# Performance work log

Hardware: AMD Instinct MI355X
Metric: run time of the kernel (lower is better)

Reference implementation:

```python
import jax, jax.numpy as jnp
import numpy as np

EPS = 1e-6

def _l2norm(t):
    # F.normalize over channel axis (axis=1) of (B, dk, L)
    n = jnp.sqrt(jnp.sum(t * t, axis=1, keepdims=True))
    return t / jnp.maximum(n, EPS)

def setup_inputs() -> dict:
    key = jax.random.key(0)
    ks = jax.random.split(key, 8)
    B, Cin, Cenc, dk, dv, H, W = 2, 64, 96, 64, 64, 96, 96
    return {
        "x": jax.random.normal(ks[0], (B, Cin, H, W), dtype=jnp.float32),
        "x_enc": jax.random.normal(ks[1], (B, Cenc, H, W), dtype=jnp.float32),
        "Wq": jax.random.normal(ks[2], (dk, Cenc), dtype=jnp.float32) * 0.05,
        "bq": jax.random.normal(ks[3], (dk,), dtype=jnp.float32) * 0.05,
        "Wk": jax.random.normal(ks[4], (dk, Cenc), dtype=jnp.float32) * 0.05,
        "bk": jax.random.normal(ks[5], (dk,), dtype=jnp.float32) * 0.05,
        "Wv": jax.random.normal(ks[6], (dv, Cin), dtype=jnp.float32) * 0.05,
        "bv": jax.random.normal(ks[7], (dv,), dtype=jnp.float32) * 0.05,
    }

def reference(x, x_enc, Wq, bq, Wk, bk, Wv, bv):
    B, _, H, W = x.shape
    L = H * W
    # 1x1 conv projections == channel matmuls, then flatten spatial dims
    Q = (jnp.einsum('bchw,kc->bkhw', x_enc, Wq) + bq[None, :, None, None]).reshape(B, -1, L)
    K = (jnp.einsum('bchw,kc->bkhw', x_enc, Wk) + bk[None, :, None, None]).reshape(B, -1, L)
    V = (jnp.einsum('bchw,kc->bkhw', x, Wv) + bv[None, :, None, None]).reshape(B, -1, L)
    # per-position L2 normalization over the dk channel axis ('l2' mode)
    Q = _l2norm(Q)
    K = _l2norm(K)
    # A[b,i,j] = sum_q Q[b,q,i] * K[b,q,j], softmax over j
    A = jax.nn.softmax(jnp.einsum('bqi,bqj->bij', Q, K), axis=-1)  # (B, L, L)
    R = jnp.einsum('bij,bvj->bvi', A, V)  # (B, dv, L)
    return R.reshape(B, -1, H, W)
```

## Files before the change

kernel.cpp:

```cpp
#include <hip/hip_runtime.h>
#include <hip/hip_bf16.h>
#include <math.h>

#define NB   2
#define CIN  64
#define CENC 96
#define DK   64
#define DV   64
#define LL   9216
#define QBLK 256
#define KVBLK 64
#define NQT  (LL/QBLK)
#define LOG2E 1.44269504088896340736f

typedef __attribute__((ext_vector_type(8)))  short short8;
typedef __attribute__((ext_vector_type(16))) float f32x16;
typedef __attribute__((ext_vector_type(2)))  unsigned int uint2v;
typedef unsigned int uint;

__device__ inline void gload16(const void* g, void* l) {
    __builtin_amdgcn_global_load_lds(
        (const __attribute__((address_space(1))) unsigned int*)g,
        (__attribute__((address_space(3))) unsigned int*)l, 16, 0, 0);
}

__device__ inline unsigned short f2bf(float f) {
    union { float f; uint u; } v; v.f = f;
    uint r = (v.u + 0x7FFFu + ((v.u >> 16) & 1u)) >> 16;
    return (unsigned short)r;
}

__device__ inline float bf2f(uint u) {
    union { uint u; float f; } c; c.u = u << 16; return c.f;
}

__device__ inline uint cvtpk(float lo, float hi) {
    uint r;
    asm("v_cvt_pk_bf16_f32 %0, %1, %2" : "=v"(r) : "v"(lo), "v"(hi));
    return r;
}

__device__ inline void plswap(uint& a, uint& b) {
#if __has_builtin(__builtin_amdgcn_permlane32_swap)
    uint2v r = __builtin_amdgcn_permlane32_swap(a, b, false, false);
    a = r.x; b = r.y;
#else
    const int lane = threadIdx.x & 63;
    uint t = (lane < 32) ? b : a;
    t = __shfl_xor(t, 32, 64);
    uint an = (lane < 32) ? a : t;
    uint bn = (lane < 32) ? t : b;
    a = an; b = bn;
#endif
}

__global__ __launch_bounds__(256) void proj_kernel(
    const float* __restrict__ x, const float* __restrict__ x_enc,
    const float* __restrict__ Wq, const float* __restrict__ bq,
    const float* __restrict__ Wk, const float* __restrict__ bk,
    const float* __restrict__ Wv, const float* __restrict__ bv,
    unsigned short* __restrict__ Qb, unsigned short* __restrict__ Kb,
    unsigned short* __restrict__ Vt, int nqk)
{
    __shared__ float sh[2 * CENC * 64];
    const int tid = threadIdx.x;

    if ((int)blockIdx.x < nqk) {
        float* Wt0 = sh;
        float* Wt1 = sh + CENC * 64;
        for (int idx = tid; idx < DK * CENC; idx += 256) {
            int k = idx / CENC, c = idx - k * CENC;
            Wt0[c * 64 + (k ^ (c & 31))] = Wq[idx];
            Wt1[c * 64 + (k ^ (c & 31))] = Wk[idx];
        }
        __syncthreads();

        const int w    = __builtin_amdgcn_readfirstlane(tid >> 6);
        const int lane = tid & 63;
        const int gw   = blockIdx.x * 4 + w;
        const int p0g  = gw * 16;
        const int b    = p0g / LL;
        const int p0   = p0g - b * LL;

        float qa[16], ka[16];
        const float bqv = bq[lane], bkv = bk[lane];
#pragma unroll
        for (int p = 0; p < 16; ++p) { qa[p] = bqv; ka[p] = bkv; }

        const float* xp = x_enc + (size_t)b * CENC * LL + p0;
#pragma unroll 4
        for (int c = 0; c < CENC; ++c) {
            const float wq = Wt0[c * 64 + (lane ^ (c & 31))];
            const float wk = Wt1[c * 64 + (lane ^ (c & 31))];
            const float* xc = xp + (size_t)c * LL;
#pragma unroll
            for (int p = 0; p < 16; ++p) {
                const float xv = xc[p];
                qa[p] = fmaf(wq, xv, qa[p]);
                ka[p] = fmaf(wk, xv, ka[p]);
            }
        }

        unsigned short* qrow = Qb + (size_t)(b * LL + p0) * 64 + lane;
        unsigned short* krow = Kb + (size_t)(b * LL + p0) * 64 + lane;
#pragma unroll
        for (int p = 0; p < 16; ++p) {
            float sq = qa[p] * qa[p];
            float sk = ka[p] * ka[p];
#pragma unroll
            for (int m = 1; m < 64; m <<= 1) {
                sq += __shfl_xor(sq, m, 64);
                sk += __shfl_xor(sk, m, 64);
            }
            qrow[(size_t)p * 64] = f2bf(qa[p] * (LOG2E / fmaxf(sqrtf(sq), 1e-6f)));
            krow[(size_t)p * 64] = f2bf(ka[p] * (1.f / fmaxf(sqrtf(sk), 1e-6f)));
        }
    } else {
        float* Wt = sh;
        unsigned short* Vsh = (unsigned short*)(sh + CIN * 64);
        for (int idx = tid; idx < DV * CIN; idx += 256) {
            int v = idx / CIN, c = idx - v * CIN;
            Wt[c * 64 + (v ^ (c & 31))] = Wv[idx];
        }
        __syncthreads();

        const int w    = __builtin_amdgcn_readfirstlane(tid >> 6);
        const int lane = tid & 63;
        const int l0g  = ((int)blockIdx.x - nqk) * 64;
        const int b    = l0g / LL;
        const int l0   = l0g - b * LL;
        const int p0   = w * 16;

        float va[16];
        const float bvv = bv[lane];
#pragma unroll
        for (int p = 0; p < 16; ++p) va[p] = bvv;

        const float* xp = x + (size_t)b * CIN * LL + l0 + p0;
#pragma unroll 4
        for (int c = 0; c < CIN; ++c) {
            const float wv = Wt[c * 64 + (lane ^ (c & 31))];
            const float* xc = xp + (size_t)c * LL;
#pragma unroll
            for (int p = 0; p < 16; ++p) va[p] = fmaf(wv, xc[p], va[p]);
        }
#pragma unroll
        for (int p = 0; p < 16; ++p) Vsh[(p0 + p) * 64 + lane] = f2bf(va[p]);
        __syncthreads();

        const int v = tid & 63, w2 = tid >> 6;
        uint pk[8];
#pragma unroll
        for (int j = 0; j < 8; ++j)
            pk[j] = (uint)Vsh[(w2 * 16 + 2 * j) * 64 + v] |
                    ((uint)Vsh[(w2 * 16 + 2 * j + 1) * 64 + v] << 16);
        uint4* dst = (uint4*)(Vt + (size_t)b * 64 * LL + (size_t)v * LL + l0 + w2 * 16);
        dst[0] = make_uint4(pk[0], pk[1], pk[2], pk[3]);
        dst[1] = make_uint4(pk[4], pk[5], pk[6], pk[7]);
    }
}

__global__ __launch_bounds__(256, 2) void flash_kernel(
    const unsigned short* __restrict__ Qb,
    const unsigned short* __restrict__ Kb,
    const unsigned short* __restrict__ Vt,
    float* __restrict__ Sp, unsigned short* __restrict__ Rp,
    int JS, int nt)
{
    __shared__ unsigned short Sh[16384];

    const int bid0  = blockIdx.x;
    const int chunk = gridDim.x >> 3;
    const int bid   = (bid0 & 7) * chunk + (bid0 >> 3);

    const int qt  = bid % NQT;
    const int js  = (bid / NQT) % JS;
    const int b   = bid / (NQT * JS);
    const int tid = threadIdx.x;
    const int w = tid >> 6, lane = tid & 63;
    const int ln = lane & 31, h = lane >> 5;
    const int i0w = qt * QBLK + w * 64;

    short8 qf[2][4];
#pragma unroll
    for (int ig = 0; ig < 2; ++ig)
#pragma unroll
        for (int kc = 0; kc < 4; ++kc)
            qf[ig][kc] = *(const short8*)(Qb + ((size_t)(b * LL + i0w + ig * 32 + ln)) * 64 + kc * 16 + h * 8);

    int aK[4];
#pragma unroll
    for (int kc = 0; kc < 4; ++kc)
        aK[kc] = ln * 128 + ((((kc << 1) + h) ^ (ln & 7)) << 4);

    const int o0 = w * 1024 + lane * 16;
    const int r0 = o0 >> 7;
    const int c0 = ((o0 >> 4) & 7) ^ (r0 & 7);

    const unsigned short* KbB = Kb + (size_t)b * LL * 64;
    const unsigned short* VtB = Vt + (size_t)b * 64 * LL;
    const int jbase = js * nt * KVBLK;

    f32x16 racc[2][2];
#pragma unroll
    for (int ig = 0; ig < 2; ++ig)
#pragma unroll
        for (int vg = 0; vg < 2; ++vg)
#pragma unroll
            for (int r = 0; r < 16; ++r) racc[ig][vg][r] = 0.f;
    float ssum[2] = {0.f, 0.f};

    gload16(KbB + (size_t)(jbase + r0) * 64 + c0 * 8, (char*)Sh + w * 1024);
    gload16(KbB + (size_t)(jbase + 32 + r0) * 64 + c0 * 8, (char*)Sh + 4096 + w * 1024);
    gload16(VtB + (size_t)r0 * LL + jbase + c0 * 8, (char*)Sh + 16384 + w * 1024);
    gload16(VtB + (size_t)(32 + r0) * LL + jbase + c0 * 8, (char*)Sh + 16384 + 4096 + w * 1024);

    const unsigned short* pK = KbB + (size_t)(jbase + KVBLK + r0) * 64 + c0 * 8;
    const unsigned short* pV = VtB + (size_t)r0 * LL + jbase + KVBLK + c0 * 8;

#define PREF(BUFOFF)                                                            \
    do {                                                                        \
        gload16(pK,                    (char*)Sh + (BUFOFF) + w * 1024);        \
        gload16(pK + 32 * 64,          (char*)Sh + (BUFOFF) + 4096 + w * 1024); \
        gload16(pV,                    (char*)Sh + 16384 + (BUFOFF) + w * 1024);\
        gload16(pV + (size_t)32 * LL,  (char*)Sh + 16384 + (BUFOFF) + 4096 + w * 1024); \
        pK += KVBLK * 64; pV += KVBLK;                                          \
    } while (0)

#define COMPUTE(BUFOFF)                                                         \
    do {                                                                        \
        _Pragma("unroll")                                                       \
        for (int jt = 0; jt < 2; ++jt) {                                        \
            f32x16 sacc[2];                                                     \
            _Pragma("unroll")                                                   \
            for (int ig = 0; ig < 2; ++ig)                                      \
                _Pragma("unroll")                                               \
                for (int r = 0; r < 16; ++r) sacc[ig][r] = 0.f;                 \
            __builtin_amdgcn_s_setprio(1);                                      \
            _Pragma("unroll")                                                   \
            for (int kc = 0; kc < 4; ++kc) {                                    \
                const short8 kf = *(const short8*)((const char*)Sh + (BUFOFF) + jt * 4096 + aK[kc]); \
                sacc[0] = __builtin_amdgcn_mfma_f32_32x32x16_bf16(kf, qf[0][kc], sacc[0], 0, 0, 0); \
                sacc[1] = __builtin_amdgcn_mfma_f32_32x32x16_bf16(kf, qf[1][kc], sacc[1], 0, 0, 0); \
            }                                                                   \
            __builtin_amdgcn_s_setprio(0);                                      \
            short8 pf[2][2];                                                    \
            _Pragma("unroll")                                                   \
            for (int ig = 0; ig < 2; ++ig) {                                    \
                _Pragma("unroll")                                               \
                for (int r = 0; r < 16; ++r) sacc[ig][r] = __builtin_amdgcn_exp2f(sacc[ig][r]); \
                float s0 = 0.f;                                                 \
                _Pragma("unroll")                                               \
                for (int r = 0; r < 16; r += 4)                                 \
                    s0 += (sacc[ig][r] + sacc[ig][r + 1]) + (sacc[ig][r + 2] + sacc[ig][r + 3]); \
                ssum[ig] += s0;                                                 \
                _Pragma("unroll")                                               \
                for (int c = 0; c < 2; ++c) {                                   \
                    uint a0 = cvtpk(sacc[ig][8 * c + 0], sacc[ig][8 * c + 1]);  \
                    uint b0 = cvtpk(sacc[ig][8 * c + 4], sacc[ig][8 * c + 5]);  \
                    uint a1 = cvtpk(sacc[ig][8 * c + 2], sacc[ig][8 * c + 3]);  \
                    uint b1 = cvtpk(sacc[ig][8 * c + 6], sacc[ig][8 * c + 7]);  \
                    plswap(a0, b0);                                             \
                    plswap(a1, b1);                                             \
                    union { uint u[4]; short8 s; } P;                           \
                    P.u[0] = a0; P.u[1] = a1; P.u[2] = b0; P.u[3] = b1;         \
                    pf[ig][c] = P.s;                                            \
                }                                                               \
            }                                                                   \
            __builtin_amdgcn_s_setprio(1);                                      \
            _Pragma("unroll")                                                   \
            for (int c = 0; c < 2; ++c) {                                       \
                const int kcv = 2 * jt + c;                                     \
                _Pragma("unroll")                                               \
                for (int vg = 0; vg < 2; ++vg) {                                \
                    const short8 vf = *(const short8*)((const char*)Sh + 16384 + (BUFOFF) + vg * 4096 + aK[kcv]); \
                    racc[0][vg] = __builtin_amdgcn_mfma_f32_32x32x16_bf16(pf[0][c], vf, racc[0][vg], 0, 0, 0); \
                    racc[1][vg] = __builtin_amdgcn_mfma_f32_32x32x16_bf16(pf[1][c], vf, racc[1][vg], 0, 0, 0); \
                }                                                               \
            }                                                                   \
            __builtin_amdgcn_s_setprio(0);                                      \
        }                                                                       \
    } while (0)

    int t = 0;
    for (; t + 2 <= nt; t += 2) {
        __syncthreads();
        PREF(8192);
        COMPUTE(0);
        __syncthreads();
        if (t + 2 < nt) PREF(0);
        COMPUTE(8192);
    }
    if (t < nt) {
        __syncthreads();
        COMPUTE(0);
    }
#undef PREF
#undef COMPUTE

#pragma unroll
    for (int ig = 0; ig < 2; ++ig) {
        float s = ssum[ig] + __shfl_xor(ssum[ig], 32, 64);
        if (h == 0) Sp[(size_t)(b * JS + js) * LL + i0w + ig * 32 + ln] = s;
    }
    const size_t rBase = (size_t)(b * JS + js) * 64;
#pragma unroll
    for (int ig = 0; ig < 2; ++ig)
#pragma unroll
        for (int vg = 0; vg < 2; ++vg) {
            unsigned short* dst = Rp + (rBase + vg * 32 + ln) * (size_t)LL + i0w + ig * 32 + 4 * h;
#pragma unroll
            for (int rr = 0; rr < 4; ++rr) {
                uint2v val;
                val.x = cvtpk(racc[ig][vg][4 * rr + 0], racc[ig][vg][4 * rr + 1]);
                val.y = cvtpk(racc[ig][vg][4 * rr + 2], racc[ig][vg][4 * rr + 3]);
                *(uint2v*)&dst[8 * rr] = val;
            }
        }
}

__global__ __launch_bounds__(256) void combine_kernel(
    const float* __restrict__ Sp, const unsigned short* __restrict__ Rp,
    float* __restrict__ out, int JS)
{
    size_t g4 = ((size_t)blockIdx.x * 256 + threadIdx.x) * 4;
    int l = (int)(g4 % LL);
    int v = (int)((g4 / LL) % 64);
    int b = (int)(g4 / ((size_t)64 * LL));
    float4 s = make_float4(0.f, 0.f, 0.f, 0.f);
    float4 r = make_float4(0.f, 0.f, 0.f, 0.f);
    for (int js = 0; js < JS; ++js) {
        const float4 sv = *(const float4*)&Sp[(size_t)(b * JS + js) * LL + l];
        const uint2v rv = *(const uint2v*)&Rp[((size_t)(b * JS + js) * 64 + v) * LL + l];
        s.x += sv.x; s.y += sv.y; s.z += sv.z; s.w += sv.w;
        r.x += bf2f(rv.x & 0xffffu); r.y += bf2f(rv.x >> 16);
        r.z += bf2f(rv.y & 0xffffu); r.w += bf2f(rv.y >> 16);
    }
    *(float4*)&out[g4] = make_float4(r.x / s.x, r.y / s.y, r.z / s.z, r.w / s.w);
}

extern "C" void kernel_launch(void* const* d_in, const int* in_sizes, int n_in,
                              void* d_out, int out_size, void* d_ws, size_t ws_size,
                              hipStream_t stream) {
    (void)in_sizes; (void)n_in; (void)out_size;
    const float* x     = (const float*)d_in[0];
    const float* x_enc = (const float*)d_in[1];
    const float* Wq    = (const float*)d_in[2];
    const float* bq    = (const float*)d_in[3];
    const float* Wk    = (const float*)d_in[4];
    const float* bk    = (const float*)d_in[5];
    const float* Wv    = (const float*)d_in[6];
    const float* bv    = (const float*)d_in[7];
    float* out = (float*)d_out;
    char* ws = (char*)d_ws;

    const size_t nBF = (size_t)NB * LL * 64 * 2;
    unsigned short* Qb = (unsigned short*)ws;
    unsigned short* Kb = (unsigned short*)(ws + nBF);
    unsigned short* Vt = (unsigned short*)(ws + 2 * nBF);

    int JS = 8;
    {
        const int cand[3] = {16, 12, 8};
        for (int ci = 0; ci < 3; ++ci) {
            JS = cand[ci];
            size_t need = 3 * nBF + (size_t)NB * JS * LL * 4 + (size_t)NB * JS * 64 * LL * 2;
            if (need <= ws_size) break;
        }
    }
    float* Sp = (float*)(ws + 3 * nBF);
    unsigned short* Rp = (unsigned short*)(ws + 3 * nBF + (size_t)NB * JS * LL * 4);
    int nt = (LL / JS) / KVBLK;

    const int nqk = NB * LL / 64;
    proj_kernel   <<<2 * nqk, 256, 0, stream>>>(x, x_enc, Wq, bq, Wk, bk, Wv, bv, Qb, Kb, Vt, nqk);
    flash_kernel  <<<NB * JS * NQT, 256, 0, stream>>>(Qb, Kb, Vt, Sp, Rp, JS, nt);
    combine_kernel<<<(NB * 64 * LL) / 1024, 256, 0, stream>>>(Sp, Rp, out, JS);
}
```

Baseline: 98.12 us.

## Double KV tile to 128 keys per stage and reduce split-K count

Raises the key/value block from 64 to 128 rows per pipeline stage, doubling the shared-memory buffers to 64 KB and processing four 32-key subtiles per stage. This halves the number of barriers and prefetch issues per block. The KV split factor drops from 16 to 12, so each block runs longer and there are fewer partial results for the combine kernel. The larger LDS footprint may limit how many blocks fit per CU, and fewer blocks in the grid lowers parallelism.

```diff
diff --git a/kernel.cpp b/kernel.cpp
--- a/kernel.cpp
+++ b/kernel.cpp
@@ -9,7 +9,7 @@
 #define DV   64
 #define LL   9216
 #define QBLK 256
-#define KVBLK 64
+#define KVBLK 128
 #define NQT  (LL/QBLK)
 #define LOG2E 1.44269504088896340736f
 
@@ -167,7 +167,7 @@
     float* __restrict__ Sp, unsigned short* __restrict__ Rp,
     int JS, int nt)
 {
-    __shared__ unsigned short Sh[16384];
+    __shared__ unsigned short Sh[32768];
 
     const int bid0  = blockIdx.x;
     const int chunk = gridDim.x >> 3;
@@ -210,76 +210,86 @@
             for (int r = 0; r < 16; ++r) racc[ig][vg][r] = 0.f;
     float ssum[2] = {0.f, 0.f};
 
-    gload16(KbB + (size_t)(jbase + r0) * 64 + c0 * 8, (char*)Sh + w * 1024);
-    gload16(KbB + (size_t)(jbase + 32 + r0) * 64 + c0 * 8, (char*)Sh + 4096 + w * 1024);
-    gload16(VtB + (size_t)r0 * LL + jbase + c0 * 8, (char*)Sh + 16384 + w * 1024);
-    gload16(VtB + (size_t)(32 + r0) * LL + jbase + c0 * 8, (char*)Sh + 16384 + 4096 + w * 1024);
+#pragma unroll
+    for (int jh = 0; jh < 2; ++jh) {
+        const int jb = jbase + jh * 64;
+        gload16(KbB + (size_t)(jb + r0) * 64 + c0 * 8,      (char*)Sh + jh * 16384 + w * 1024);
+        gload16(KbB + (size_t)(jb + 32 + r0) * 64 + c0 * 8, (char*)Sh + jh * 16384 + 4096 + w * 1024);
+        gload16(VtB + (size_t)r0 * LL + jb + c0 * 8,        (char*)Sh + 32768 + jh * 16384 + w * 1024);
+        gload16(VtB + (size_t)(32 + r0) * LL + jb + c0 * 8, (char*)Sh + 32768 + jh * 16384 + 4096 + w * 1024);
+    }
 
     const unsigned short* pK = KbB + (size_t)(jbase + KVBLK + r0) * 64 + c0 * 8;
     const unsigned short* pV = VtB + (size_t)r0 * LL + jbase + KVBLK + c0 * 8;
 
-#define PREF(BUFOFF)                                                            \
-    do {                                                                        \
-        gload16(pK,                    (char*)Sh + (BUFOFF) + w * 1024);        \
-        gload16(pK + 32 * 64,          (char*)Sh + (BUFOFF) + 4096 + w * 1024); \
-        gload16(pV,                    (char*)Sh + 16384 + (BUFOFF) + w * 1024);\
-        gload16(pV + (size_t)32 * LL,  (char*)Sh + 16384 + (BUFOFF) + 4096 + w * 1024); \
-        pK += KVBLK * 64; pV += KVBLK;                                          \
+#define PREF(BUFOFF)                                                                  \
+    do {                                                                              \
+        _Pragma("unroll")                                                             \
+        for (int jh = 0; jh < 2; ++jh) {                                              \
+            gload16(pK + jh * 4096,        (char*)Sh + jh * 16384 + (BUFOFF) + w * 1024); \
+            gload16(pK + jh * 4096 + 2048, (char*)Sh + jh * 16384 + (BUFOFF) + 4096 + w * 1024); \
+            gload16(pV + jh * 64,                   (char*)Sh + 32768 + jh * 16384 + (BUFOFF) + w * 1024); \
+            gload16(pV + jh * 64 + (size_t)32 * LL, (char*)Sh + 32768 + jh * 16384 + (BUFOFF) + 4096 + w * 1024); \
+        }                                                                             \
+        pK += (size_t)KVBLK * 64; pV += KVBLK;                                        \
     } while (0)
 
-#define COMPUTE(BUFOFF)                                                         \
-    do {                                                                        \
-        _Pragma("unroll")                                                       \
-        for (int jt = 0; jt < 2; ++jt) {                                        \
-            f32x16 sacc[2];                                                     \
-            _Pragma("unroll")                                                   \
-            for (int ig = 0; ig < 2; ++ig)                                      \
-                _Pragma("unroll")                                               \
-                for (int r = 0; r < 16; ++r) sacc[ig][r] = 0.f;                 \
-            __builtin_amdgcn_s_setprio(1);                                      \
-            _Pragma("unroll")                                                   \
-            for (int kc = 0; kc < 4; ++kc) {                                    \
-                const short8 kf = *(const short8*)((const char*)Sh + (BUFOFF) + jt * 4096 + aK[kc]); \
+#define COMPUTE(BUFOFF)                                                               \
+    do {                                                                              \
+        _Pragma("unroll")                                                             \
+        for (int jt = 0; jt < 4; ++jt) {                                              \
+            const int jh = jt >> 1;                                                   \
+            const char* KlB = (const char*)Sh + jh * 16384 + (BUFOFF) + (jt & 1) * 4096; \
+            const char* VlB = (const char*)Sh + 32768 + jh * 16384 + (BUFOFF);        \
+            f32x16 sacc[2];                                                           \
+            _Pragma("unroll")                                                         \
+            for (int ig = 0; ig < 2; ++ig)                                            \
+                _Pragma("unroll")                                                     \
+                for (int r = 0; r < 16; ++r) sacc[ig][r] = 0.f;                       \
+            __builtin_amdgcn_s_setprio(1);                                            \
+            _Pragma("unroll")                                                         \
+            for (int kc = 0; kc < 4; ++kc) {                                          \
+                const short8 kf = *(const short8*)(KlB + aK[kc]);                     \
                 sacc[0] = __builtin_amdgcn_mfma_f32_32x32x16_bf16(kf, qf[0][kc], sacc[0], 0, 0, 0); \
                 sacc[1] = __builtin_amdgcn_mfma_f32_32x32x16_bf16(kf, qf[1][kc], sacc[1], 0, 0, 0); \
-            }                                                                   \
-            __builtin_amdgcn_s_setprio(0);                                      \
-            short8 pf[2][2];                                                    \
-            _Pragma("unroll")                                                   \
-            for (int ig = 0; ig < 2; ++ig) {                                    \
-                _Pragma("unroll")                                               \
+            }                                                                         \
+            __builtin_amdgcn_s_setprio(0);                                            \
+            short8 pf[2][2];                                                          \
+            _Pragma("unroll")                                                         \
+            for (int ig = 0; ig < 2; ++ig) {                                          \
+                _Pragma("unroll")                                                     \
                 for (int r = 0; r < 16; ++r) sacc[ig][r] = __builtin_amdgcn_exp2f(sacc[ig][r]); \
-                float s0 = 0.f;                                                 \
-                _Pragma("unroll")                                               \
-                for (int r = 0; r < 16; r += 4)                                 \
+                float s0 = 0.f;                                                       \
+                _Pragma("unroll")                                                     \
+                for (int r = 0; r < 16; r += 4)                                       \
                     s0 += (sacc[ig][r] + sacc[ig][r + 1]) + (sacc[ig][r + 2] + sacc[ig][r + 3]); \
-                ssum[ig] += s0;                                                 \
-                _Pragma("unroll")                                               \
-                for (int c = 0; c < 2; ++c) {                                   \
-                    uint a0 = cvtpk(sacc[ig][8 * c + 0], sacc[ig][8 * c + 1]);  \
-                    uint b0 = cvtpk(sacc[ig][8 * c + 4], sacc[ig][8 * c + 5]);  \
-                    uint a1 = cvtpk(sacc[ig][8 * c + 2], sacc[ig][8 * c + 3]);  \
-                    uint b1 = cvtpk(sacc[ig][8 * c + 6], sacc[ig][8 * c + 7]);  \
-                    plswap(a0, b0);                                             \
-                    plswap(a1, b1);                                             \
-                    union { uint u[4]; short8 s; } P;                           \
-                    P.u[0] = a0; P.u[1] = a1; P.u[2] = b0; P.u[3] = b1;         \
-                    pf[ig][c] = P.s;                                            \
-                }                                                               \
-            }                                                                   \
-            __builtin_amdgcn_s_setprio(1);                                      \
-            _Pragma("unroll")                                                   \
-            for (int c = 0; c < 2; ++c) {                                       \
-                const int kcv = 2 * jt + c;                                     \
-                _Pragma("unroll")                                               \
-                for (int vg = 0; vg < 2; ++vg) {                                \
-                    const short8 vf = *(const short8*)((const char*)Sh + 16384 + (BUFOFF) + vg * 4096 + aK[kcv]); \
+                ssum[ig] += s0;                                                       \
+                _Pragma("unroll")                                                     \
+                for (int c = 0; c < 2; ++c) {                                         \
+                    uint a0 = cvtpk(sacc[ig][8 * c + 0], sacc[ig][8 * c + 1]);        \
+                    uint b0 = cvtpk(sacc[ig][8 * c + 4], sacc[ig][8 * c + 5]);        \
+                    uint a1 = cvtpk(sacc[ig][8 * c + 2], sacc[ig][8 * c + 3]);        \
+                    uint b1 = cvtpk(sacc[ig][8 * c + 6], sacc[ig][8 * c + 7]);        \
+                    plswap(a0, b0);                                                   \
+                    plswap(a1, b1);                                                   \
+                    union { uint u[4]; short8 s; } P;                                 \
+                    P.u[0] = a0; P.u[1] = a1; P.u[2] = b0; P.u[3] = b1;               \
+                    pf[ig][c] = P.s;                                                  \
+                }                                                                     \
+            }                                                                         \
+            __builtin_amdgcn_s_setprio(1);                                            \
+            _Pragma("unroll")                                                         \
+            for (int c = 0; c < 2; ++c) {                                             \
+                const int kl = (jt & 1) * 2 + c;                                      \
+                _Pragma("unroll")                                                     \
+                for (int vg = 0; vg < 2; ++vg) {                                      \
+                    const short8 vf = *(const short8*)(VlB + vg * 4096 + aK[kl]);     \
                     racc[0][vg] = __builtin_amdgcn_mfma_f32_32x32x16_bf16(pf[0][c], vf, racc[0][vg], 0, 0, 0); \
                     racc[1][vg] = __builtin_amdgcn_mfma_f32_32x32x16_bf16(pf[1][c], vf, racc[1][vg], 0, 0, 0); \
-                }                                                               \
-            }                                                                   \
-            __builtin_amdgcn_s_setprio(0);                                      \
-        }                                                                       \
+                }                                                                     \
+            }                                                                         \
+            __builtin_amdgcn_s_setprio(0);                                            \
+        }                                                                             \
     } while (0)
 
     int t = 0;
@@ -359,9 +369,9 @@
     unsigned short* Kb = (unsigned short*)(ws + nBF);
     unsigned short* Vt = (unsigned short*)(ws + 2 * nBF);
 
-    int JS = 8;
+    int JS = 12;
     {
-        const int cand[3] = {16, 12, 8};
+        const int cand[3] = {12, 8, 4};
         for (int ci = 0; ci < 3; ++ci) {
             JS = cand[ci];
             size_t need = 3 * nBF + (size_t)NB * JS * LL * 4 + (size_t)NB * JS * 64 * LL * 2;
```

Result: slower. 102.0 us (+4.0%).
